# Optimization experiments

Hardware: AMD Instinct MI355X
Metric: run time of the kernel (lower is better)

## Reference

```python
import jax, jax.numpy as jnp
import numpy as np

B, T, TKV, D, H = 4, 2048, 512, 1024, 16
HD = D // H  # 64
HIDDEN = ((int(D * 4 * 2 / 3) + 7) // 8) * 8  # 2736
EPS = 1e-6


def setup_inputs() -> dict:
    key = jax.random.key(0)
    ks = jax.random.split(key, 16)
    x = jax.random.normal(ks[0], (B, T, D), jnp.float32)
    memory = jax.random.normal(ks[1], (B, TKV, D), jnp.float32)
    # RoPE frequencies: (T, HD//2, 2) = (cos, sin)
    inv_freq = 1.0 / (10000.0 ** (jnp.arange(0, HD, 2, dtype=jnp.float32) / HD))
    angles = jnp.arange(T, dtype=jnp.float32)[:, None] * inv_freq[None, :]
    freqs_cis = jnp.stack([jnp.cos(angles), jnp.sin(angles)], axis=-1)
    # causal mask (T, T): 0 on/below diag, -inf above
    causal_mask = jnp.where(jnp.tril(jnp.ones((T, T), bool)), 0.0, -jnp.inf).astype(jnp.float32)
    s = 0.02
    w = lambda k, i, o: jax.random.normal(k, (i, o), jnp.float32) * s  # stored as (in, out)
    return {
        'x': x, 'memory': memory, 'freqs_cis': freqs_cis, 'causal_mask': causal_mask,
        'sa_wq': w(ks[2], D, D), 'sa_wk': w(ks[3], D, D), 'sa_wv': w(ks[4], D, D), 'sa_wo': w(ks[5], D, D),
        'ca_wq': w(ks[6], D, D), 'ca_wk': w(ks[7], D, D), 'ca_wv': w(ks[8], D, D), 'ca_wo': w(ks[9], D, D),
        'w1': w(ks[10], D, HIDDEN), 'w3': w(ks[11], D, HIDDEN), 'w2': w(ks[12], HIDDEN, D),
        'g_sa': jnp.ones((D,), jnp.float32), 'g_ca': jnp.ones((D,), jnp.float32), 'g_ffn': jnp.ones((D,), jnp.float32),
    }


def rmsnorm(x, g):
    return x * jax.lax.rsqrt(jnp.mean(x * x, axis=-1, keepdims=True) + EPS) * g


def apply_rope(t, f):
    # t: (B, H, T, HD); f: (T, HD//2, 2)
    tr = t.reshape(*t.shape[:-1], HD // 2, 2)
    a, b = tr[..., 0], tr[..., 1]
    cos, sin = f[None, None, :, :, 0], f[None, None, :, :, 1]
    out = jnp.stack([a * cos - b * sin, a * sin + b * cos], axis=-1)
    return out.reshape(t.shape)


def heads(x, w):
    # (B, S, D) @ (D, D) -> (B, H, S, HD)
    b, s, _ = x.shape
    return (x @ w).reshape(b, s, H, HD).transpose(0, 2, 1, 3)


def attention(xq, kv, wq, wk, wv, wo, freqs=None, mask=None):
    q, k, v = heads(xq, wq), heads(kv, wk), heads(kv, wv)
    if freqs is not None:
        q, k = apply_rope(q, freqs), apply_rope(k, freqs)
    attn = jnp.einsum('bhqd,bhkd->bhqk', q, k) * (HD ** -0.5)
    if mask is not None:
        attn = attn + mask
    attn = jax.nn.softmax(attn, axis=-1)
    out = jnp.einsum('bhqk,bhkd->bhqd', attn, v)
    out = out.transpose(0, 2, 1, 3).reshape(xq.shape[0], xq.shape[1], D)
    return out @ wo


def reference(x, memory, freqs_cis, causal_mask,
              sa_wq, sa_wk, sa_wv, sa_wo,
              ca_wq, ca_wk, ca_wv, ca_wo,
              w1, w2, w3, g_sa, g_ca, g_ffn):
    x = rmsnorm(x + attention(x, x, sa_wq, sa_wk, sa_wv, sa_wo, freqs=freqs_cis, mask=causal_mask), g_sa)
    x = rmsnorm(x + attention(x, memory, ca_wq, ca_wk, ca_wv, ca_wo), g_ca)
    ffn = (jax.nn.silu(x @ w1) * (x @ w3)) @ w2
    x = rmsnorm(x + ffn, g_ffn)
    return x
```

## Files before the change

### kernel.cpp

```cpp
#include <hip/hip_runtime.h>
#include <hip/hip_bf16.h>

typedef __attribute__((ext_vector_type(8))) short s16x8;
typedef __attribute__((ext_vector_type(4))) float f32x4;
typedef __attribute__((ext_vector_type(16))) float f32x16;
typedef unsigned short u16;
typedef unsigned int u32;
typedef unsigned long long u64;

#define MFMA(a,b,c) __builtin_amdgcn_mfma_f32_16x16x32_bf16(a,b,c,0,0,0)
#define MFMA32(a,b,c) __builtin_amdgcn_mfma_f32_32x32x16_bf16(a,b,c,0,0,0)

constexpr int B_ = 4, T_ = 2048, TKV_ = 512, D_ = 1024, H_ = 16, HD_ = 64;
constexpr int HID_ = 2736, HIDP_ = 2816;

__device__ __forceinline__ float bf2f(u16 x) {
    union { float f; u32 u; } c; c.u = ((u32)x) << 16; return c.f;
}
__device__ __forceinline__ u16 f2bf(float f) {
    union { float f; u32 u; } c; c.f = f;
    u32 r = c.u + 0x7fffu + ((c.u >> 16) & 1u);
    return (u16)(r >> 16);
}

__device__ __forceinline__ void gload16(const void* g, void* l) {
    __builtin_amdgcn_global_load_lds(
        (const __attribute__((address_space(1))) u32*)g,
        (__attribute__((address_space(3))) u32*)l, 16, 0, 0);
}

__global__ __launch_bounds__(256) void wt_cast(const float* __restrict__ W, u16* __restrict__ WT,
                                               int K, int N, int Kp, int Np) {
    __shared__ float t[32][33];
    int tid = threadIdx.x;
    int tx = tid & 31, ty = tid >> 5;
    int n0 = blockIdx.x * 32, k0 = blockIdx.y * 32;
#pragma unroll
    for (int i = 0; i < 4; ++i) {
        int kk = k0 + ty + i * 8, nn = n0 + tx;
        t[ty + i * 8][tx] = (kk < K && nn < N) ? W[(size_t)kk * N + nn] : 0.f;
    }
    __syncthreads();
#pragma unroll
    for (int i = 0; i < 4; ++i) {
        int nn = n0 + ty + i * 8, kk = k0 + tx;
        WT[(size_t)nn * Kp + kk] = f2bf(t[tx][ty + i * 8]);
    }
}

__global__ __launch_bounds__(256) void cast_bf16(const float* __restrict__ in, u16* __restrict__ out, int n4) {
    int i = blockIdx.x * 256 + threadIdx.x;
    if (i >= n4) return;
    float4 v = ((const float4*)in)[i];
    u64 pk = (u64)f2bf(v.x) | ((u64)f2bf(v.y) << 16) | ((u64)f2bf(v.z) << 32) | ((u64)f2bf(v.w) << 48);
    ((u64*)out)[i] = pk;
}

__global__ __launch_bounds__(256) void gemm_bf16(const u16* __restrict__ A, const u16* __restrict__ Bt,
                                                 void* __restrict__ C, const u16* __restrict__ mul,
                                                 int M, int N, int K, int mode) {
    __shared__ __align__(16) u16 As[128 * 64];
    __shared__ __align__(16) u16 Bs[128 * 64];
    const int tid = threadIdx.x;
    const int lane = tid & 63, wid = tid >> 6;
    const int wr = wid >> 1, wc = wid & 1;
    const int li = lane & 15, g = lane >> 4;
    const int tn = N >> 7;
    const int m0 = (blockIdx.x / tn) * 128, n0 = (blockIdx.x % tn) * 128;

    f32x4 acc[4][4] = {};
    const int rowst = tid >> 3;
    const int colb = (tid & 7) * 16;

    for (int k0 = 0; k0 < K; k0 += 64) {
#pragma unroll
        for (int i = 0; i < 4; ++i) {
            gload16((const char*)A + (((size_t)(m0 + i * 32 + rowst)) * K + k0) * 2 + colb,
                    (char*)As + i * 4096 + wid * 1024);
            gload16((const char*)Bt + (((size_t)(n0 + i * 32 + rowst)) * K + k0) * 2 + colb,
                    (char*)Bs + i * 4096 + wid * 1024);
        }
        __syncthreads();
#pragma unroll
        for (int kk = 0; kk < 2; ++kk) {
            s16x8 aF[4], bF[4];
#pragma unroll
            for (int m = 0; m < 4; ++m) aF[m] = *(const s16x8*)&As[(wr * 64 + m * 16 + li) * 64 + kk * 32 + g * 8];
#pragma unroll
            for (int n = 0; n < 4; ++n) bF[n] = *(const s16x8*)&Bs[(wc * 64 + n * 16 + li) * 64 + kk * 32 + g * 8];
#pragma unroll
            for (int m = 0; m < 4; ++m)
#pragma unroll
                for (int n = 0; n < 4; ++n)
                    acc[m][n] = MFMA(aF[m], bF[n], acc[m][n]);
        }
        __syncthreads();
    }

#pragma unroll
    for (int m = 0; m < 4; ++m)
#pragma unroll
        for (int n = 0; n < 4; ++n)
#pragma unroll
            for (int r = 0; r < 4; ++r) {
                size_t row = m0 + wr * 64 + m * 16 + g * 4 + r;
                size_t col = n0 + wc * 64 + n * 16 + li;
                size_t idx = row * N + col;
                float v = acc[m][n][r];
                if (mode == 0) {
                    ((float*)C)[idx] = v;
                } else if (mode == 1) {
                    ((u16*)C)[idx] = f2bf(v);
                } else if (mode == 2) {
                    float sg = 1.f / (1.f + __expf(-v));
                    ((u16*)C)[idx] = f2bf(v * sg);
                } else if (mode == 3) {
                    float h = bf2f(mul[idx]);
                    ((u16*)C)[idx] = f2bf(v * h);
                } else {
                    ((u16*)C)[idx] = f2bf(v * 0.125f);
                }
            }
}

__global__ __launch_bounds__(256) void rope_qk(u16* __restrict__ q, u16* __restrict__ k,
                                               const float* __restrict__ fr) {
    size_t idx = (size_t)blockIdx.x * 256 + threadIdx.x;
    int i = (int)(idx & 31);
    int h = (int)((idx >> 5) & 15);
    size_t bt = idx >> 9;
    int t = (int)(bt & (T_ - 1));
    float2 cs = ((const float2*)fr)[t * 32 + i];
    size_t off = bt * D_ + h * 64 + 2 * i;
    {
        u32* p = (u32*)(q + off);
        u32 w = *p;
        float a = bf2f((u16)(w & 0xffff)), b = bf2f((u16)(w >> 16));
        *p = (u32)f2bf((a * cs.x - b * cs.y) * 0.125f) | ((u32)f2bf((a * cs.y + b * cs.x) * 0.125f) << 16);
    }
    {
        u32* p = (u32*)(k + off);
        u32 w = *p;
        float a = bf2f((u16)(w & 0xffff)), b = bf2f((u16)(w >> 16));
        *p = (u32)f2bf(a * cs.x - b * cs.y) | ((u32)f2bf(a * cs.y + b * cs.x) << 16);
    }
}

__global__ __launch_bounds__(256) void vtrans(const u16* __restrict__ v, u16* __restrict__ vT, int Tk) {
    __shared__ u16 tile[32][34];
    int bh = blockIdx.x;
    int t0 = blockIdx.y * 32, d0 = blockIdx.z * 32;
    int b = bh >> 4, h = bh & 15;
    int tid = threadIdx.x;
    int tx = tid & 31, ty = tid >> 5;
#pragma unroll
    for (int i = 0; i < 4; ++i)
        tile[ty + i * 8][tx] = v[((size_t)b * Tk + t0 + ty + i * 8) * D_ + h * 64 + d0 + tx];
    __syncthreads();
#pragma unroll
    for (int i = 0; i < 4; ++i)
        vT[((size_t)bh * 64 + d0 + ty + i * 8) * Tk + t0 + tx] = tile[tx][ty + i * 8];
}

__device__ __forceinline__ void attn32(const u16* __restrict__ qh, const u16* __restrict__ kh,
                                       const u16* __restrict__ vh, u16* __restrict__ oh,
                                       int q0, int nkb, int Tk, int causal, int lq, int hi) {
    const u16* qb = qh + (size_t)(q0 + lq) * D_;
    s16x8 qf[4];
#pragma unroll
    for (int c = 0; c < 4; ++c) qf[c] = *(const s16x8*)&qb[c * 16 + hi * 8];

    f32x16 o0 = {}, o1 = {};
    float mr = -1e30f, lr = 0.f;

    for (int kb = 0; kb < nkb; ++kb) {
        const int ks = kb * 32;
        f32x16 s = {};
        const u16* kp = kh + (size_t)(ks + lq) * D_ + hi * 8;
#pragma unroll
        for (int c = 0; c < 4; ++c) {
            s16x8 kf = *(const s16x8*)&kp[c * 16];
            s = MFMA32(kf, qf[c], s);
        }
        if (causal && kb == nkb - 1) {
#pragma unroll
            for (int r = 0; r < 16; ++r) {
                int kl = (r & 3) + 8 * (r >> 2) + 4 * hi;
                if (kl > lq) s[r] = -1e30f;
            }
        }
        float bm = fmaxf(fmaxf(fmaxf(s[0], s[1]), fmaxf(s[2], s[3])),
                         fmaxf(fmaxf(s[4], s[5]), fmaxf(s[6], s[7])));
        float bm2 = fmaxf(fmaxf(fmaxf(s[8], s[9]), fmaxf(s[10], s[11])),
                          fmaxf(fmaxf(s[12], s[13]), fmaxf(s[14], s[15])));
        bm = fmaxf(bm, bm2);
        bm = fmaxf(bm, __shfl_xor(bm, 32));
        float mn = fmaxf(mr, bm);
        float sc = __expf(mr - mn);
        mr = mn;
        float p[16];
        float rs = 0.f;
#pragma unroll
        for (int r = 0; r < 16; ++r) { p[r] = __expf(s[r] - mn); rs += p[r]; }
        rs += __shfl_xor(rs, 32);
        lr = lr * sc + rs;
#pragma unroll
        for (int r = 0; r < 16; ++r) { o0[r] *= sc; o1[r] *= sc; }

        u32 pk[8];
#pragma unroll
        for (int i = 0; i < 8; ++i)
            pk[i] = (u32)f2bf(p[2 * i]) | ((u32)f2bf(p[2 * i + 1]) << 16);
        u32 e1 = __shfl_xor(hi ? pk[0] : pk[2], 32);
        u32 e2 = __shfl_xor(hi ? pk[1] : pk[3], 32);
        u32 e3 = __shfl_xor(hi ? pk[4] : pk[6], 32);
        u32 e4 = __shfl_xor(hi ? pk[5] : pk[7], 32);
        union { s16x8 v; u32 w[4]; } pf0, pf1;
        pf0.w[0] = hi ? e1 : pk[0];
        pf0.w[1] = hi ? e2 : pk[1];
        pf0.w[2] = hi ? pk[2] : e1;
        pf0.w[3] = hi ? pk[3] : e2;
        pf1.w[0] = hi ? e3 : pk[4];
        pf1.w[1] = hi ? e4 : pk[5];
        pf1.w[2] = hi ? pk[6] : e3;
        pf1.w[3] = hi ? pk[7] : e4;

        const u16* v0 = vh + (size_t)lq * Tk + ks + hi * 8;
        const u16* v1 = vh + (size_t)(32 + lq) * Tk + ks + hi * 8;
        o0 = MFMA32(*(const s16x8*)&v0[0],  pf0.v, o0);
        o0 = MFMA32(*(const s16x8*)&v0[16], pf1.v, o0);
        o1 = MFMA32(*(const s16x8*)&v1[0],  pf0.v, o1);
        o1 = MFMA32(*(const s16x8*)&v1[16], pf1.v, o1);
    }

    float inv = 1.f / lr;
    u16* ob = oh + (size_t)(q0 + lq) * D_;
#pragma unroll
    for (int r = 0; r < 16; ++r) {
        int hd = (r & 3) + 8 * (r >> 2) + 4 * hi;
        ob[hd] = f2bf(o0[r] * inv);
        ob[hd + 32] = f2bf(o1[r] * inv);
    }
}

__global__ __launch_bounds__(256) void attn_causal32(const u16* __restrict__ q, const u16* __restrict__ k,
                                                     const u16* __restrict__ vT, u16* __restrict__ o,
                                                     int Tq, int Tk) {
    const int lane = threadIdx.x & 63, wid = threadIdx.x >> 6;
    const int lq = lane & 31, hi = lane >> 5;
    const int ntile = Tq / 32;
    const int ppb = (ntile / 2) / 4;
    const int bh = blockIdx.x / ppb;
    const int p = (blockIdx.x % ppb) * 4 + wid;
    const int b = bh >> 4, h = bh & 15;

    const u16* qh = q + ((size_t)b * Tq) * D_ + h * 64;
    const u16* kh = k + ((size_t)b * Tk) * D_ + h * 64;
    const u16* vh = vT + ((size_t)bh * 64) * Tk;
    u16* oh = o + ((size_t)b * Tq) * D_ + h * 64;

    const int tA = p, tB = ntile - 1 - p;
    attn32(qh, kh, vh, oh, tA * 32, tA + 1, Tk, 1, lq, hi);
    attn32(qh, kh, vh, oh, tB * 32, tB + 1, Tk, 1, lq, hi);
}

__global__ __launch_bounds__(256) void attn_plain32(const u16* __restrict__ q, const u16* __restrict__ k,
                                                    const u16* __restrict__ vT, u16* __restrict__ o,
                                                    int Tq, int Tk) {
    const int lane = threadIdx.x & 63, wid = threadIdx.x >> 6;
    const int lq = lane & 31, hi = lane >> 5;
    const int tpb = (Tq / 32) / 4;
    const int bh = blockIdx.x / tpb;
    const int qt = (blockIdx.x % tpb) * 4 + wid;
    const int b = bh >> 4, h = bh & 15;

    const u16* qh = q + ((size_t)b * Tq) * D_ + h * 64;
    const u16* kh = k + ((size_t)b * Tk) * D_ + h * 64;
    const u16* vh = vT + ((size_t)bh * 64) * Tk;
    u16* oh = o + ((size_t)b * Tq) * D_ + h * 64;

    attn32(qh, kh, vh, oh, qt * 32, Tk / 32, Tk, 0, lq, hi);
}

__global__ __launch_bounds__(256) void addnorm(const float* __restrict__ xa, const float* __restrict__ xb,
                                               const float* __restrict__ gg, float* __restrict__ fo,
                                               u16* __restrict__ bo) {
    int row = blockIdx.x, tid = threadIdx.x;
    float4 a = ((const float4*)(xa + (size_t)row * D_))[tid];
    float4 b = ((const float4*)(xb + (size_t)row * D_))[tid];
    float vx = a.x + b.x, vy = a.y + b.y, vz = a.z + b.z, vw = a.w + b.w;
    float ss = vx * vx + vy * vy + vz * vz + vw * vw;
    ss += __shfl_xor(ss, 1);
    ss += __shfl_xor(ss, 2);
    ss += __shfl_xor(ss, 4);
    ss += __shfl_xor(ss, 8);
    ss += __shfl_xor(ss, 16);
    ss += __shfl_xor(ss, 32);
    __shared__ float red[4];
    int lane = tid & 63, wid = tid >> 6;
    if (lane == 0) red[wid] = ss;
    __syncthreads();
    float tot = red[0] + red[1] + red[2] + red[3];
    float s = rsqrtf(tot * (1.0f / D_) + 1e-6f);
    float4 gv = ((const float4*)gg)[tid];
    float yx = vx * s * gv.x, yy = vy * s * gv.y, yz = vz * s * gv.z, yw = vw * s * gv.w;
    if (fo) {
        float4 o4; o4.x = yx; o4.y = yy; o4.z = yz; o4.w = yw;
        ((float4*)(fo + (size_t)row * D_))[tid] = o4;
    }
    if (bo) {
        u64 pk = (u64)f2bf(yx) | ((u64)f2bf(yy) << 16) | ((u64)f2bf(yz) << 32) | ((u64)f2bf(yw) << 48);
        ((u64*)(bo + (size_t)row * D_))[tid] = pk;
    }
}

extern "C" void kernel_launch(void* const* d_in, const int* in_sizes, int n_in,
                              void* d_out, int out_size, void* d_ws, size_t ws_size,
                              hipStream_t stream) {
    const float* x    = (const float*)d_in[0];
    const float* mem  = (const float*)d_in[1];
    const float* fr   = (const float*)d_in[2];
    const float* wsaq = (const float*)d_in[4];
    const float* wsak = (const float*)d_in[5];
    const float* wsav = (const float*)d_in[6];
    const float* wsao = (const float*)d_in[7];
    const float* wcaq = (const float*)d_in[8];
    const float* wcak = (const float*)d_in[9];
    const float* wcav = (const float*)d_in[10];
    const float* wcao = (const float*)d_in[11];
    const float* w1   = (const float*)d_in[12];
    const float* w3   = (const float*)d_in[13];
    const float* w2   = (const float*)d_in[14];
    const float* g_sa = (const float*)d_in[15];
    const float* g_ca = (const float*)d_in[16];
    const float* g_ff = (const float*)d_in[17];
    float* outF = (float*)d_out;

    char* p = (char*)d_ws;
    auto alloc = [&](size_t bytes) { char* r = p; p += (bytes + 255) & ~(size_t)255; return r; };
    const size_t DD2 = (size_t)1024 * 1024 * 2;
    u16* saqT = (u16*)alloc(DD2);
    u16* sakT = (u16*)alloc(DD2);
    u16* savT = (u16*)alloc(DD2);
    u16* saoT = (u16*)alloc(DD2);
    u16* caqT = (u16*)alloc(DD2);
    u16* cakT = (u16*)alloc(DD2);
    u16* cavT = (u16*)alloc(DD2);
    u16* caoT = (u16*)alloc(DD2);
    u16* w1T  = (u16*)alloc((size_t)HIDP_ * 1024 * 2);
    u16* w3T  = (u16*)alloc((size_t)HIDP_ * 1024 * 2);
    u16* w2T  = (u16*)alloc((size_t)1024 * HIDP_ * 2);
    u16* Ab   = (u16*)alloc((size_t)8192 * 1024 * 2);
    u16* memb = (u16*)alloc((size_t)2048 * 1024 * 2);
    u16* qb   = (u16*)alloc((size_t)8192 * 1024 * 2);
    u16* kb   = (u16*)alloc((size_t)8192 * 1024 * 2);
    u16* vb   = (u16*)alloc((size_t)8192 * 1024 * 2);
    u16* vtb  = (u16*)alloc((size_t)8192 * 1024 * 2);
    u16* ob   = (u16*)alloc((size_t)8192 * 1024 * 2);
    float* Pf = (float*)alloc((size_t)8192 * 1024 * 4);
    float* Rf = (float*)alloc((size_t)8192 * 1024 * 4);
    u16* Hb   = (u16*)alloc((size_t)8192 * HIDP_ * 2);

    dim3 blk(256);

    wt_cast<<<dim3(32, 32), blk, 0, stream>>>(wsaq, saqT, 1024, 1024, 1024, 1024);
    wt_cast<<<dim3(32, 32), blk, 0, stream>>>(wsak, sakT, 1024, 1024, 1024, 1024);
    wt_cast<<<dim3(32, 32), blk, 0, stream>>>(wsav, savT, 1024, 1024, 1024, 1024);
    wt_cast<<<dim3(32, 32), blk, 0, stream>>>(wsao, saoT, 1024, 1024, 1024, 1024);
    wt_cast<<<dim3(32, 32), blk, 0, stream>>>(wcaq, caqT, 1024, 1024, 1024, 1024);
    wt_cast<<<dim3(32, 32), blk, 0, stream>>>(wcak, cakT, 1024, 1024, 1024, 1024);
    wt_cast<<<dim3(32, 32), blk, 0, stream>>>(wcav, cavT, 1024, 1024, 1024, 1024);
    wt_cast<<<dim3(32, 32), blk, 0, stream>>>(wcao, caoT, 1024, 1024, 1024, 1024);
    wt_cast<<<dim3(88, 32), blk, 0, stream>>>(w1, w1T, 1024, HID_, 1024, HIDP_);
    wt_cast<<<dim3(88, 32), blk, 0, stream>>>(w3, w3T, 1024, HID_, 1024, HIDP_);
    wt_cast<<<dim3(32, 88), blk, 0, stream>>>(w2, w2T, HID_, 1024, HIDP_, 1024);

    cast_bf16<<<8192, blk, 0, stream>>>(x, Ab, 2097152);
    cast_bf16<<<2048, blk, 0, stream>>>(mem, memb, 524288);

    gemm_bf16<<<512, blk, 0, stream>>>(Ab, saqT, qb, nullptr, 8192, 1024, 1024, 1);
    gemm_bf16<<<512, blk, 0, stream>>>(Ab, sakT, kb, nullptr, 8192, 1024, 1024, 1);
    gemm_bf16<<<512, blk, 0, stream>>>(Ab, savT, vb, nullptr, 8192, 1024, 1024, 1);
    rope_qk<<<16384, blk, 0, stream>>>(qb, kb, fr);
    vtrans<<<dim3(64, 64, 2), blk, 0, stream>>>(vb, vtb, 2048);
    attn_causal32<<<512, blk, 0, stream>>>(qb, kb, vtb, ob, 2048, 2048);
    gemm_bf16<<<512, blk, 0, stream>>>(ob, saoT, Pf, nullptr, 8192, 1024, 1024, 0);
    addnorm<<<8192, blk, 0, stream>>>(x, Pf, g_sa, Rf, Ab);

    gemm_bf16<<<512, blk, 0, stream>>>(Ab, caqT, qb, nullptr, 8192, 1024, 1024, 4);
    gemm_bf16<<<128, blk, 0, stream>>>(memb, cakT, kb, nullptr, 2048, 1024, 1024, 1);
    gemm_bf16<<<128, blk, 0, stream>>>(memb, cavT, vb, nullptr, 2048, 1024, 1024, 1);
    vtrans<<<dim3(64, 16, 2), blk, 0, stream>>>(vb, vtb, 512);
    attn_plain32<<<1024, blk, 0, stream>>>(qb, kb, vtb, ob, 2048, 512);
    gemm_bf16<<<512, blk, 0, stream>>>(ob, caoT, Pf, nullptr, 8192, 1024, 1024, 0);
    addnorm<<<8192, blk, 0, stream>>>(Rf, Pf, g_ca, Rf, Ab);

    gemm_bf16<<<64 * 22, blk, 0, stream>>>(Ab, w1T, Hb, nullptr, 8192, HIDP_, 1024, 2);
    gemm_bf16<<<64 * 22, blk, 0, stream>>>(Ab, w3T, Hb, Hb, 8192, HIDP_, 1024, 3);
    gemm_bf16<<<512, blk, 0, stream>>>(Hb, w2T, Pf, nullptr, 8192, 1024, HIDP_, 0);
    addnorm<<<8192, blk, 0, stream>>>(Rf, Pf, g_ff, outF, nullptr);
}
```

Measured before the change: 956.7 us.

## Double-buffer GEMM LDS tiles and remap blocks across XCDs

```diff
diff --git a/kernel.cpp b/kernel.cpp
--- a/kernel.cpp
+++ b/kernel.cpp
@@ -58,36 +58,54 @@
 
 __global__ __launch_bounds__(256) void gemm_bf16(const u16* __restrict__ A, const u16* __restrict__ Bt,
                                                  void* __restrict__ C, const u16* __restrict__ mul,
-                                                 int M, int N, int K, int mode) {
-    __shared__ __align__(16) u16 As[128 * 64];
-    __shared__ __align__(16) u16 Bs[128 * 64];
+                                                 int M, int N, int K, int mode, int nwg) {
+    __shared__ __align__(16) u16 As[2][128 * 64];
+    __shared__ __align__(16) u16 Bs[2][128 * 64];
     const int tid = threadIdx.x;
     const int lane = tid & 63, wid = tid >> 6;
     const int wr = wid >> 1, wc = wid & 1;
     const int li = lane & 15, g = lane >> 4;
+
+    int bid = (int)blockIdx.x;
+    bid = (bid & 7) * (nwg >> 3) + (bid >> 3);
+
     const int tn = N >> 7;
-    const int m0 = (blockIdx.x / tn) * 128, n0 = (blockIdx.x % tn) * 128;
-
-    f32x4 acc[4][4] = {};
+    const int m0 = (bid / tn) * 128, n0 = (bid % tn) * 128;
+
     const int rowst = tid >> 3;
     const int colb = (tid & 7) * 16;
-
-    for (int k0 = 0; k0 < K; k0 += 64) {
-#pragma unroll
-        for (int i = 0; i < 4; ++i) {
-            gload16((const char*)A + (((size_t)(m0 + i * 32 + rowst)) * K + k0) * 2 + colb,
-                    (char*)As + i * 4096 + wid * 1024);
-            gload16((const char*)Bt + (((size_t)(n0 + i * 32 + rowst)) * K + k0) * 2 + colb,
-                    (char*)Bs + i * 4096 + wid * 1024);
+    const char* ga = (const char*)A + ((size_t)(m0 + rowst) * K) * 2 + colb;
+    const char* gb = (const char*)Bt + ((size_t)(n0 + rowst) * K) * 2 + colb;
+    const size_t rstride = (size_t)32 * K * 2;
+
+    f32x4 acc[4][4] = {};
+    const int nt = K >> 6;
+
+#pragma unroll
+    for (int i = 0; i < 4; ++i) {
+        gload16(ga + i * rstride, (char*)As[0] + i * 4096 + wid * 1024);
+        gload16(gb + i * rstride, (char*)Bs[0] + i * 4096 + wid * 1024);
+    }
+    __syncthreads();
+
+    int cur = 0;
+    for (int t = 0; t < nt; ++t) {
+        if (t + 1 < nt) {
+            const char* gan = ga + (size_t)(t + 1) * 128;
+            const char* gbn = gb + (size_t)(t + 1) * 128;
+#pragma unroll
+            for (int i = 0; i < 4; ++i) {
+                gload16(gan + i * rstride, (char*)As[cur ^ 1] + i * 4096 + wid * 1024);
+                gload16(gbn + i * rstride, (char*)Bs[cur ^ 1] + i * 4096 + wid * 1024);
+            }
         }
-        __syncthreads();
 #pragma unroll
         for (int kk = 0; kk < 2; ++kk) {
             s16x8 aF[4], bF[4];
 #pragma unroll
-            for (int m = 0; m < 4; ++m) aF[m] = *(const s16x8*)&As[(wr * 64 + m * 16 + li) * 64 + kk * 32 + g * 8];
-#pragma unroll
-            for (int n = 0; n < 4; ++n) bF[n] = *(const s16x8*)&Bs[(wc * 64 + n * 16 + li) * 64 + kk * 32 + g * 8];
+            for (int m = 0; m < 4; ++m) aF[m] = *(const s16x8*)&As[cur][(wr * 64 + m * 16 + li) * 64 + kk * 32 + g * 8];
+#pragma unroll
+            for (int n = 0; n < 4; ++n) bF[n] = *(const s16x8*)&Bs[cur][(wc * 64 + n * 16 + li) * 64 + kk * 32 + g * 8];
 #pragma unroll
             for (int m = 0; m < 4; ++m)
 #pragma unroll
@@ -95,6 +113,7 @@
                     acc[m][n] = MFMA(aF[m], bF[n], acc[m][n]);
         }
         __syncthreads();
+        cur ^= 1;
     }
 
 #pragma unroll
@@ -378,25 +397,25 @@
     cast_bf16<<<8192, blk, 0, stream>>>(x, Ab, 2097152);
     cast_bf16<<<2048, blk, 0, stream>>>(mem, memb, 524288);
 
-    gemm_bf16<<<512, blk, 0, stream>>>(Ab, saqT, qb, nullptr, 8192, 1024, 1024, 1);
-    gemm_bf16<<<512, blk, 0, stream>>>(Ab, sakT, kb, nullptr, 8192, 1024, 1024, 1);
-    gemm_bf16<<<512, blk, 0, stream>>>(Ab, savT, vb, nullptr, 8192, 1024, 1024, 1);
+    gemm_bf16<<<512, blk, 0, stream>>>(Ab, saqT, qb, nullptr, 8192, 1024, 1024, 1, 512);
+    gemm_bf16<<<512, blk, 0, stream>>>(Ab, sakT, kb, nullptr, 8192, 1024, 1024, 1, 512);
+    gemm_bf16<<<512, blk, 0, stream>>>(Ab, savT, vb, nullptr, 8192, 1024, 1024, 1, 512);
     rope_qk<<<16384, blk, 0, stream>>>(qb, kb, fr);
     vtrans<<<dim3(64, 64, 2), blk, 0, stream>>>(vb, vtb, 2048);
     attn_causal32<<<512, blk, 0, stream>>>(qb, kb, vtb, ob, 2048, 2048);
-    gemm_bf16<<<512, blk, 0, stream>>>(ob, saoT, Pf, nullptr, 8192, 1024, 1024, 0);
+    gemm_bf16<<<512, blk, 0, stream>>>(ob, saoT, Pf, nullptr, 8192, 1024, 1024, 0, 512);
     addnorm<<<8192, blk, 0, stream>>>(x, Pf, g_sa, Rf, Ab);
 
-    gemm_bf16<<<512, blk, 0, stream>>>(Ab, caqT, qb, nullptr, 8192, 1024, 1024, 4);
-    gemm_bf16<<<128, blk, 0, stream>>>(memb, cakT, kb, nullptr, 2048, 1024, 1024, 1);
-    gemm_bf16<<<128, blk, 0, stream>>>(memb, cavT, vb, nullptr, 2048, 1024, 1024, 1);
+    gemm_bf16<<<512, blk, 0, stream>>>(Ab, caqT, qb, nullptr, 8192, 1024, 1024, 4, 512);
+    gemm_bf16<<<128, blk, 0, stream>>>(memb, cakT, kb, nullptr, 2048, 1024, 1024, 1, 128);
+    gemm_bf16<<<128, blk, 0, stream>>>(memb, cavT, vb, nullptr, 2048, 1024, 1024, 1, 128);
     vtrans<<<dim3(64, 16, 2), blk, 0, stream>>>(vb, vtb, 512);
     attn_plain32<<<1024, blk, 0, stream>>>(qb, kb, vtb, ob, 2048, 512);
-    gemm_bf16<<<512, blk, 0, stream>>>(ob, caoT, Pf, nullptr, 8192, 1024, 1024, 0);
+    gemm_bf16<<<512, blk, 0, stream>>>(ob, caoT, Pf, nullptr, 8192, 1024, 1024, 0, 512);
     addnorm<<<8192, blk, 0, stream>>>(Rf, Pf, g_ca, Rf, Ab);
 
-    gemm_bf16<<<64 * 22, blk, 0, stream>>>(Ab, w1T, Hb, nullptr, 8192, HIDP_, 1024, 2);
-    gemm_bf16<<<64 * 22, blk, 0, stream>>>(Ab, w3T, Hb, Hb, 8192, HIDP_, 1024, 3);
-    gemm_bf16<<<512, blk, 0, stream>>>(Hb, w2T, Pf, nullptr, 8192, 1024, HIDP_, 0);
+    gemm_bf16<<<64 * 22, blk, 0, stream>>>(Ab, w1T, Hb, nullptr, 8192, HIDP_, 1024, 2, 64 * 22);
+    gemm_bf16<<<64 * 22, blk, 0, stream>>>(Ab, w3T, Hb, Hb, 8192, HIDP_, 1024, 3, 64 * 22);
+    gemm_bf16<<<512, blk, 0, stream>>>(Hb, w2T, Pf, nullptr, 8192, 1024, HIDP_, 0, 512);
     addnorm<<<8192, blk, 0, stream>>>(Rf, Pf, g_ff, outF, nullptr);
 }
```

After: 945.1 us. No clear change (-1.2%).
